# Performance work log

Measured on AMD Instinct MI355X. Metric: run time of the kernel, lower is better.

Reference implementation:

```python
import jax, jax.numpy as jnp
import numpy as np

N, L, D, HEADS = 32, 128, 128, 4
B = 64
MHSA_RESIDUAL = False  # module default


def setup_inputs() -> dict:
    key = jax.random.key(0)
    ks = jax.random.split(key, 21)
    g = lambda k, shape, s=0.05: jax.random.normal(k, shape, dtype=jnp.float32) * s
    return {
        "X": jax.random.normal(ks[0], (B, L, N), dtype=jnp.float32),
        # per-variable encoder LSTM weights, stacked over N (torch gate order i,f,g,o)
        "enc_Wih": g(ks[1], (N, 4 * D)),        # input size is 1 -> (4d,1) squeezed
        "enc_Whh": g(ks[2], (N, 4 * D, D)),
        "enc_bih": g(ks[3], (N, 4 * D)),
        "enc_bhh": g(ks[4], (N, 4 * D)),
        "pool_w": g(ks[5], (N, D)),
        "pool_b": g(ks[6], (N,)),
        # nn.MultiheadAttention packed in-proj + out-proj
        "Wqkv": g(ks[7], (3 * D, D)),
        "bqkv": g(ks[8], (3 * D,)),
        "Wo": g(ks[9], (D, D)),
        "bo": g(ks[10], (D,)),
        # per-variable decoder: init_h/init_c Linear(d, d), LSTM, out Linear(d,1)
        "dec_ih_W": g(ks[11], (N, D, D)),
        "dec_ih_b": g(ks[12], (N, D)),
        "dec_ic_W": g(ks[13], (N, D, D)),
        "dec_ic_b": g(ks[14], (N, D)),
        "dec_Wih": g(ks[15], (N, 4 * D)),       # unused at runtime: decoder input is zeros
        "dec_Whh": g(ks[16], (N, 4 * D, D)),
        "dec_bih": g(ks[17], (N, 4 * D)),
        "dec_bhh": g(ks[18], (N, 4 * D)),
        "dec_out_W": g(ks[19], (N, D)),
        "dec_out_b": g(ks[20], (N,)),
    }


def _lstm_cell(pre, c):
    i, f, g, o = jnp.split(pre, 4, axis=-1)
    c_new = jax.nn.sigmoid(f) * c + jax.nn.sigmoid(i) * jnp.tanh(g)
    h_new = jax.nn.sigmoid(o) * jnp.tanh(c_new)
    return h_new, c_new


def reference(X, enc_Wih, enc_Whh, enc_bih, enc_bhh, pool_w, pool_b,
              Wqkv, bqkv, Wo, bo,
              dec_ih_W, dec_ih_b, dec_ic_W, dec_ic_b,
              dec_Wih, dec_Whh, dec_bih, dec_bhh, dec_out_W, dec_out_b):
    Bx = X.shape[0]
    # ---- N per-variable LSTM encoders, batched over the N axis ----
    x_enc = jnp.transpose(X[:, :L - 1, :], (1, 2, 0))  # (L-1, N, B)
    h0 = jnp.zeros((N, Bx, D), X.dtype)

    def enc_step(carry, x_t):
        h, c = carry
        pre = (x_t[..., None] * enc_Wih[:, None, :]
               + jnp.einsum('nbd,ngd->nbg', h, enc_Whh)
               + (enc_bih + enc_bhh)[:, None, :])
        h, c = _lstm_cell(pre, c)
        return (h, c), h

    _, H = jax.lax.scan(enc_step, (h0, h0), x_enc)  # (L-1, N, B, D)

    # temporal attention pooling (softmax over time)
    s = jnp.einsum('tnbd,nd->tnb', H, pool_w) + pool_b[None, :, None]
    a = jax.nn.softmax(s, axis=0)
    C = jnp.transpose(jnp.einsum('tnb,tnbd->nbd', a, H), (1, 0, 2))  # (B, N, D)

    # ---- MHSA over the variable axis ----
    qkv = C @ Wqkv.T + bqkv  # (B, N, 3D)
    q, k, v = jnp.split(qkv, 3, axis=-1)
    dh = D // HEADS
    split = lambda t: t.reshape(Bx, N, HEADS, dh).transpose(0, 2, 1, 3)  # (B,h,N,dh)
    q, k, v = split(q), split(k), split(v)
    attn = jax.nn.softmax(jnp.einsum('bhqd,bhkd->bhqk', q, k) / jnp.sqrt(jnp.float32(dh)), axis=-1)
    A = jnp.einsum('bhqk,bhkd->bhqd', attn, v).transpose(0, 2, 1, 3).reshape(Bx, N, D)
    A = A @ Wo.T + bo
    C_star = C + A if MHSA_RESIDUAL else A  # (B, N, D)

    # ---- N per-variable LSTM decoders, batched over the N axis ----
    cs = jnp.transpose(C_star, (1, 0, 2))  # (N, B, D)
    h = jnp.tanh(jnp.einsum('nbd,ned->nbe', cs, dec_ih_W) + dec_ih_b[:, None, :])
    c = jnp.tanh(jnp.einsum('nbd,ned->nbe', cs, dec_ic_W) + dec_ic_b[:, None, :])

    def dec_step(carry, _):
        h, c = carry
        # decoder input is identically zero -> W_ih contributes nothing
        pre = jnp.einsum('nbd,ngd->nbg', h, dec_Whh) + (dec_bih + dec_bhh)[:, None, :]
        h, c = _lstm_cell(pre, c)
        return (h, c), h

    _, Y = jax.lax.scan(dec_step, (h, c), None, length=L)  # (L, N, B, D)
    O = jnp.einsum('lnbd,nd->lnb', Y, dec_out_W) + dec_out_b[None, :, None]  # (L, N, B)
    recon = jnp.transpose(O[:L - 1], (2, 0, 1))  # (B, L-1, N)
    pred = O[L - 1].T                             # (B, N)
    return recon, pred, C_star
```

## Files before the change

### kernel.cpp

```cpp
#include <hip/hip_runtime.h>


typedef _Float16 h8  __attribute__((ext_vector_type(8)));
typedef _Float16 h4v __attribute__((ext_vector_type(4)));
typedef float    f4  __attribute__((ext_vector_type(4)));
typedef float    f2v __attribute__((ext_vector_type(2)));

#define DI __device__ __forceinline__

constexpr int NV  = 32;
constexpr int LT  = 128;
constexpr int DH  = 128;
constexpr int GG  = 4 * DH;
constexpr int BR  = 8;
constexpr int NW  = 8;
constexpr int TPB = NW * 64;
constexpr int HSTR = DH + 8;
constexpr float LOG2E = 1.4426950408889634f;

DI float rcp_(float x) { return __builtin_amdgcn_rcpf(x); }
DI float ex2_(float x) { return __builtin_amdgcn_exp2f(x); }

DI float tanh_(float x) {
    float xc = fminf(fmaxf(x, -20.0f), 20.0f);
    float E = ex2_(2.0f * LOG2E * xc);
    return (E - 1.0f) * rcp_(E + 1.0f);
}

DI float lstm_cell(float iv, float fv, float gv, float ov, float& c) {
    float Ai = ex2_(iv);
    float Af = ex2_(fv);
    float Bg = ex2_(gv);
    float ai1 = 1.0f + Ai, af1 = 1.0f + Af, bg1 = 1.0f + Bg;
    float P = ai1 * bg1;
    float N = fmaf(c, P, (Bg - 1.0f) * af1);
    c = N * rcp_(P * af1);
    float cc = fminf(fmaxf(c, -20.0f), 20.0f);
    float Ec = ex2_(2.0f * LOG2E * cc);
    float Eo = ex2_(ov);
    return (Ec - 1.0f) * rcp_((1.0f + Eo) * (1.0f + Ec));
}

DI h8 cvt8(f4 a, f4 b) {
    h8 r;
    r[0] = (_Float16)a[0]; r[1] = (_Float16)a[1];
    r[2] = (_Float16)a[2]; r[3] = (_Float16)a[3];
    r[4] = (_Float16)b[0]; r[5] = (_Float16)b[1];
    r[6] = (_Float16)b[2]; r[7] = (_Float16)b[3];
    return r;
}
DI h8 cvt8s(f4 a, f4 b, float s) {
    h8 r;
    r[0] = (_Float16)(a[0] * s); r[1] = (_Float16)(a[1] * s);
    r[2] = (_Float16)(a[2] * s); r[3] = (_Float16)(a[3] * s);
    r[4] = (_Float16)(b[0] * s); r[5] = (_Float16)(b[1] * s);
    r[6] = (_Float16)(b[2] * s); r[7] = (_Float16)(b[3] * s);
    return r;
}

__constant__ float GSC[4] = {-LOG2E, -LOG2E, 2.0f * LOG2E, -LOG2E};

__global__ __launch_bounds__(TPB, 2)
void enc_kernel(const float* __restrict__ X,
                const float* __restrict__ Wih,
                const float* __restrict__ Whh,
                const float* __restrict__ bih,
                const float* __restrict__ bhh,
                const float* __restrict__ poolw,
                float* __restrict__ Cout)
{
    const int n    = blockIdx.x & 31;
    const int b0   = (blockIdx.x >> 5) * BR;
    const int tid  = threadIdx.x;
    const int wv   = tid >> 6;
    const int lane = tid & 63;
    const int quad = lane >> 4;
    const int l16  = lane & 15;
    const int dmy  = wv * 16 + l16;

    __shared__ _Float16 hbuf[2][16 * HSTR];
    __shared__ float xs[(LT - 1) * BR];
    __shared__ float pfin[2][BR];

    h8 Wf[4][4];
    float wihr[4];
    f4 bsp[4];
#pragma unroll
    for (int g4 = 0; g4 < 4; ++g4) {
        const float s = GSC[g4];
        const int g = g4 * DH + dmy;
        const float* wrow = Whh + (size_t)(n * GG + g) * DH;
#pragma unroll
        for (int kc = 0; kc < 4; ++kc) {
            f4 w0 = *(const f4*)(wrow + kc * 32 + quad * 8);
            f4 w1 = *(const f4*)(wrow + kc * 32 + quad * 8 + 4);
            Wf[g4][kc] = cvt8s(w0, w1, s);
        }
        wihr[g4] = Wih[n * GG + g] * s;
        const float bb = (bih[n * GG + g] + bhh[n * GG + g]) * s;
        bsp[g4] = (f4){bb, bb, bb, bb};
    }
    h8 Bp[4];
#pragma unroll
    for (int kc = 0; kc < 4; ++kc) {
        if (l16 == 0) {
            f4 p0 = *(const f4*)(poolw + n * DH + kc * 32 + quad * 8);
            f4 p1 = *(const f4*)(poolw + n * DH + kc * 32 + quad * 8 + 4);
            Bp[kc] = cvt8s(p0, p1, LOG2E);
        } else {
            Bp[kc] = (h8)(_Float16)0.0f;
        }
    }

    for (int i = tid; i < (LT - 1) * BR; i += TPB)
        xs[i] = X[((size_t)(b0 + (i & 7)) * LT + (i >> 3)) * NV + n];
    for (int i = tid; i < 2 * 16 * HSTR; i += TPB)
        ((_Float16*)hbuf)[i] = (_Float16)0.0f;
    __syncthreads();

    float cst[2]   = {0.f, 0.f};
    float lsum[2]  = {0.f, 0.f};
    float acc[2]   = {0.f, 0.f};
    float hprev[2] = {0.f, 0.f};

    for (int t = 0; t < LT - 1; ++t) {
        const _Float16* hb = hbuf[t & 1];
        h8 a[4];
#pragma unroll
        for (int kc = 0; kc < 4; ++kc)
            a[kc] = *(const h8*)(hb + l16 * HSTR + kc * 32 + quad * 8);

        f4 pre[4];
#pragma unroll
        for (int g4 = 0; g4 < 4; ++g4)
            pre[g4] = __builtin_amdgcn_mfma_f32_16x16x32_f16(
                a[0], Wf[g4][0], bsp[g4], 0, 0, 0);
#pragma unroll
        for (int kc = 1; kc < 4; ++kc)
#pragma unroll
            for (int g4 = 0; g4 < 4; ++g4)
                pre[g4] = __builtin_amdgcn_mfma_f32_16x16x32_f16(
                    a[kc], Wf[g4][kc], pre[g4], 0, 0, 0);

        if (wv == 0) {
            f4 sp = {0.f, 0.f, 0.f, 0.f};
#pragma unroll
            for (int kc = 0; kc < 4; ++kc)
                sp = __builtin_amdgcn_mfma_f32_16x16x32_f16(a[kc], Bp[kc], sp, 0, 0, 0);
            if (l16 == 0) {
                pfin[t & 1][quad * 2 + 0] = ex2_(sp[0]);
                pfin[t & 1][quad * 2 + 1] = ex2_(sp[1]);
            }
        }

        const f2v xv = *(const f2v*)(xs + t * BR + quad * 2);
        float hv[2];
#pragma unroll
        for (int r = 0; r < 2; ++r) {
            hv[r] = lstm_cell(fmaf(xv[r], wihr[0], pre[0][r]),
                              fmaf(xv[r], wihr[1], pre[1][r]),
                              fmaf(xv[r], wihr[2], pre[2][r]),
                              fmaf(xv[r], wihr[3], pre[3][r]), cst[r]);
        }

        _Float16* hn = hbuf[(t + 1) & 1];
#pragma unroll
        for (int r = 0; r < 2; ++r)
            hn[(quad * 4 + r) * HSTR + dmy] = (_Float16)hv[r];
        __syncthreads();

        if (t > 0) {
#pragma unroll
            for (int r = 0; r < 2; ++r) {
                const float p = pfin[t & 1][quad * 2 + r];
                lsum[r] += p;
                acc[r] = fmaf(p, hprev[r], acc[r]);
            }
        }
#pragma unroll
        for (int r = 0; r < 2; ++r) hprev[r] = hv[r];
    }

    if (wv == 0) {
        const _Float16* hb = hbuf[(LT - 1) & 1];
        h8 a[4];
#pragma unroll
        for (int kc = 0; kc < 4; ++kc)
            a[kc] = *(const h8*)(hb + l16 * HSTR + kc * 32 + quad * 8);
        f4 sp = {0.f, 0.f, 0.f, 0.f};
#pragma unroll
        for (int kc = 0; kc < 4; ++kc)
            sp = __builtin_amdgcn_mfma_f32_16x16x32_f16(a[kc], Bp[kc], sp, 0, 0, 0);
        if (l16 == 0) {
            pfin[(LT - 1) & 1][quad * 2 + 0] = ex2_(sp[0]);
            pfin[(LT - 1) & 1][quad * 2 + 1] = ex2_(sp[1]);
        }
    }
    __syncthreads();
#pragma unroll
    for (int r = 0; r < 2; ++r) {
        const float p = pfin[(LT - 1) & 1][quad * 2 + r];
        lsum[r] += p;
        acc[r] = fmaf(p, hprev[r], acc[r]);
    }
#pragma unroll
    for (int r = 0; r < 2; ++r) {
        const int b = b0 + quad * 2 + r;
        Cout[((size_t)b * NV + n) * DH + dmy] = acc[r] * rcp_(lsum[r]);
    }
}

constexpr int CS2 = DH + 8;
constexpr int QS  = 40;

__global__ __launch_bounds__(256)
void attn_kernel(const float* __restrict__ Cin,
                 const float* __restrict__ Wqkv,
                 const float* __restrict__ bqkv,
                 float* __restrict__ Astage)
{
    const int b    = blockIdx.x >> 2;
    const int hh   = blockIdx.x & 3;
    const int tid  = threadIdx.x;
    const int wv   = tid >> 6;
    const int lane = tid & 63;
    const int quad = lane >> 4;
    const int l16  = lane & 15;

    __shared__ _Float16 Cb[NV][CS2];
    __shared__ _Float16 qs[NV][QS], ks[NV][QS], vT[NV][QS];
    __shared__ float    S[NV][NV + 1];
    __shared__ _Float16 P[NV][QS];

    for (int i = tid; i < NV * DH / 4; i += 256) {
        const int nn = i >> 5, d4 = (i & 31) * 4;
        f4 v = *(const f4*)(Cin + ((size_t)b * NV + nn) * DH + d4);
        h4v hv4;
        hv4[0] = (_Float16)v[0]; hv4[1] = (_Float16)v[1];
        hv4[2] = (_Float16)v[2]; hv4[3] = (_Float16)v[3];
        *(h4v*)(&Cb[nn][d4]) = hv4;
    }
    __syncthreads();

    const int m0 = (wv >> 1) * 16;
    const int n0 = (wv & 1) * 16;

    h8 a[4];
#pragma unroll
    for (int kc = 0; kc < 4; ++kc)
        a[kc] = *(const h8*)(&Cb[m0 + l16][kc * 32 + quad * 8]);

#pragma unroll
    for (int mat = 0; mat < 3; ++mat) {
        const int rbase = mat * DH + hh * 32;
        const float* wrow = Wqkv + (size_t)(rbase + n0 + l16) * DH;
        const float bias  = bqkv[rbase + n0 + l16];
        f4 acc = {bias, bias, bias, bias};
#pragma unroll
        for (int kc = 0; kc < 4; ++kc) {
            f4 w0 = *(const f4*)(wrow + kc * 32 + quad * 8);
            f4 w1 = *(const f4*)(wrow + kc * 32 + quad * 8 + 4);
            acc = __builtin_amdgcn_mfma_f32_16x16x32_f16(a[kc], cvt8(w0, w1), acc, 0, 0, 0);
        }
#pragma unroll
        for (int r = 0; r < 4; ++r) {
            const int tok = m0 + quad * 4 + r, col = n0 + l16;
            if (mat == 0)      qs[tok][col] = (_Float16)acc[r];
            else if (mat == 1) ks[tok][col] = (_Float16)acc[r];
            else               vT[col][tok] = (_Float16)acc[r];
        }
    }
    __syncthreads();

    {
        h8 aq = *(const h8*)(&qs[m0 + l16][quad * 8]);
        h8 bk = *(const h8*)(&ks[n0 + l16][quad * 8]);
        f4 sc = {0.f, 0.f, 0.f, 0.f};
        sc = __builtin_amdgcn_mfma_f32_16x16x32_f16(aq, bk, sc, 0, 0, 0);
#pragma unroll
        for (int r = 0; r < 4; ++r)
            S[m0 + quad * 4 + r][n0 + l16] = sc[r] * 0.17677669529663687f;
    }
    __syncthreads();

    if (tid < NV) {
        float mx = -1e30f;
        for (int j = 0; j < NV; ++j) mx = fmaxf(mx, S[tid][j]);
        float l = 0.0f;
        float p[NV];
#pragma unroll
        for (int j = 0; j < NV; ++j) {
            p[j] = ex2_(LOG2E * (S[tid][j] - mx));
            l += p[j];
        }
        const float rl = rcp_(l);
#pragma unroll
        for (int j = 0; j < NV; ++j) P[tid][j] = (_Float16)(p[j] * rl);
    }
    __syncthreads();

    {
        h8 ap = *(const h8*)(&P[m0 + l16][quad * 8]);
        h8 bv = *(const h8*)(&vT[n0 + l16][quad * 8]);
        f4 av = {0.f, 0.f, 0.f, 0.f};
        av = __builtin_amdgcn_mfma_f32_16x16x32_f16(ap, bv, av, 0, 0, 0);
#pragma unroll
        for (int r = 0; r < 4; ++r) {
            const int tok = m0 + quad * 4 + r;
            Astage[((size_t)b * NV + tok) * DH + hh * 32 + n0 + l16] = av[r];
        }
    }
}

__global__ __launch_bounds__(256)
void outproj_kernel(const float* __restrict__ Wo,
                    const float* __restrict__ bo,
                    float* __restrict__ AC)
{
    const int mb   = blockIdx.x * 16;
    const int tid  = threadIdx.x;
    const int wv   = tid >> 6;
    const int lane = tid & 63;
    const int quad = lane >> 4;
    const int l16  = lane & 15;

    __shared__ _Float16 As[16][HSTR];

    for (int i = tid; i < 16 * DH / 4; i += 256) {
        const int rr = i >> 5, d4 = (i & 31) * 4;
        f4 v = *(const f4*)(AC + ((size_t)(mb + rr)) * DH + d4);
        h4v hv4;
        hv4[0] = (_Float16)v[0]; hv4[1] = (_Float16)v[1];
        hv4[2] = (_Float16)v[2]; hv4[3] = (_Float16)v[3];
        *(h4v*)(&As[rr][d4]) = hv4;
    }
    __syncthreads();

    h8 a[4];
#pragma unroll
    for (int kc = 0; kc < 4; ++kc)
        a[kc] = *(const h8*)(&As[l16][kc * 32 + quad * 8]);

#pragma unroll
    for (int i = 0; i < 2; ++i) {
        const int n0 = (wv * 2 + i) * 16;
        const float* wrow = Wo + (size_t)(n0 + l16) * DH;
        const float bias  = bo[n0 + l16];
        f4 acc = {bias, bias, bias, bias};
#pragma unroll
        for (int kc = 0; kc < 4; ++kc) {
            f4 w0 = *(const f4*)(wrow + kc * 32 + quad * 8);
            f4 w1 = *(const f4*)(wrow + kc * 32 + quad * 8 + 4);
            acc = __builtin_amdgcn_mfma_f32_16x16x32_f16(a[kc], cvt8(w0, w1), acc, 0, 0, 0);
        }
#pragma unroll
        for (int r = 0; r < 4; ++r)
            AC[((size_t)(mb + quad * 4 + r)) * DH + n0 + l16] = acc[r];
    }
}

__global__ __launch_bounds__(TPB, 2)
void dec_kernel(const float* __restrict__ Cstar,
                const float* __restrict__ ihW,
                const float* __restrict__ ihb,
                const float* __restrict__ icW,
                const float* __restrict__ icb,
                const float* __restrict__ Whh,
                const float* __restrict__ bih,
                const float* __restrict__ bhh,
                const float* __restrict__ outW,
                const float* __restrict__ outb,
                float* __restrict__ recon,
                float* __restrict__ pred)
{
    const int n    = blockIdx.x & 31;
    const int b0   = (blockIdx.x >> 5) * BR;
    const int tid  = threadIdx.x;
    const int wv   = tid >> 6;
    const int lane = tid & 63;
    const int quad = lane >> 4;
    const int l16  = lane & 15;
    const int dmy  = wv * 16 + l16;

    __shared__ _Float16 hbuf[2][16 * HSTR];
    __shared__ float obuf[LT - 1][BR];

    h8 Wf[4][4];
    f4 bsp[4];
#pragma unroll
    for (int g4 = 0; g4 < 4; ++g4) {
        const float s = GSC[g4];
        const int g = g4 * DH + dmy;
        const float* wrow = Whh + (size_t)(n * GG + g) * DH;
#pragma unroll
        for (int kc = 0; kc < 4; ++kc) {
            f4 w0 = *(const f4*)(wrow + kc * 32 + quad * 8);
            f4 w1 = *(const f4*)(wrow + kc * 32 + quad * 8 + 4);
            Wf[g4][kc] = cvt8s(w0, w1, s);
        }
        const float bb = (bih[n * GG + g] + bhh[n * GG + g]) * s;
        bsp[g4] = (f4){bb, bb, bb, bb};
    }
    h8 Bo[4];
#pragma unroll
    for (int kc = 0; kc < 4; ++kc) {
        if (l16 == 0) {
            f4 p0 = *(const f4*)(outW + n * DH + kc * 32 + quad * 8);
            f4 p1 = *(const f4*)(outW + n * DH + kc * 32 + quad * 8 + 4);
            Bo[kc] = cvt8(p0, p1);
        } else {
            Bo[kc] = (h8)(_Float16)0.0f;
        }
    }
    const float ob = outb[n];

    for (int i = tid; i < 2 * 16 * HSTR; i += TPB)
        ((_Float16*)hbuf)[i] = (_Float16)0.0f;
    __syncthreads();
    if (tid < 256) {
        const int j = tid >> 5, d4 = (tid & 31) * 4;
        const int row = (j >> 1) * 4 + (j & 1);
        f4 v = *(const f4*)(Cstar + ((size_t)(b0 + j) * NV + n) * DH + d4);
        h4v hv4;
        hv4[0] = (_Float16)v[0]; hv4[1] = (_Float16)v[1];
        hv4[2] = (_Float16)v[2]; hv4[3] = (_Float16)v[3];
        *(h4v*)(&hbuf[0][row * HSTR + d4]) = hv4;
    }
    __syncthreads();

    float cst[2], hv0[2];
    {
        h8 a[4];
#pragma unroll
        for (int kc = 0; kc < 4; ++kc)
            a[kc] = *(const h8*)(hbuf[0] + l16 * HSTR + kc * 32 + quad * 8);
        const float bh = ihb[n * DH + dmy];
        const float bc = icb[n * DH + dmy];
        f4 Ph = {bh, bh, bh, bh};
        f4 Pc = {bc, bc, bc, bc};
        const float* hrow = ihW + (size_t)(n * DH + dmy) * DH;
        const float* crow = icW + (size_t)(n * DH + dmy) * DH;
#pragma unroll
        for (int kc = 0; kc < 4; ++kc) {
            f4 w0 = *(const f4*)(hrow + kc * 32 + quad * 8);
            f4 w1 = *(const f4*)(hrow + kc * 32 + quad * 8 + 4);
            Ph = __builtin_amdgcn_mfma_f32_16x16x32_f16(a[kc], cvt8(w0, w1), Ph, 0, 0, 0);
            f4 u0 = *(const f4*)(crow + kc * 32 + quad * 8);
            f4 u1 = *(const f4*)(crow + kc * 32 + quad * 8 + 4);
            Pc = __builtin_amdgcn_mfma_f32_16x16x32_f16(a[kc], cvt8(u0, u1), Pc, 0, 0, 0);
        }
#pragma unroll
        for (int r = 0; r < 2; ++r) {
            hv0[r] = tanh_(Ph[r]);
            cst[r] = tanh_(Pc[r]);
        }
    }
    __syncthreads();
#pragma unroll
    for (int r = 0; r < 2; ++r)
        hbuf[0][(quad * 4 + r) * HSTR + dmy] = (_Float16)hv0[r];
    __syncthreads();

    for (int t = 0; t < LT; ++t) {
        const _Float16* hb = hbuf[t & 1];
        h8 a[4];
#pragma unroll
        for (int kc = 0; kc < 4; ++kc)
            a[kc] = *(const h8*)(hb + l16 * HSTR + kc * 32 + quad * 8);

        f4 pre[4];
#pragma unroll
        for (int g4 = 0; g4 < 4; ++g4)
            pre[g4] = __builtin_amdgcn_mfma_f32_16x16x32_f16(
                a[0], Wf[g4][0], bsp[g4], 0, 0, 0);
#pragma unroll
        for (int kc = 1; kc < 4; ++kc)
#pragma unroll
            for (int g4 = 0; g4 < 4; ++g4)
                pre[g4] = __builtin_amdgcn_mfma_f32_16x16x32_f16(
                    a[kc], Wf[g4][kc], pre[g4], 0, 0, 0);

        if (wv == 0 && t > 0) {
            f4 so = {0.f, 0.f, 0.f, 0.f};
#pragma unroll
            for (int kc = 0; kc < 4; ++kc)
                so = __builtin_amdgcn_mfma_f32_16x16x32_f16(a[kc], Bo[kc], so, 0, 0, 0);
            if (l16 == 0) {
                obuf[t - 1][quad * 2 + 0] = so[0] + ob;
                obuf[t - 1][quad * 2 + 1] = so[1] + ob;
            }
        }

        float hv[2];
#pragma unroll
        for (int r = 0; r < 2; ++r)
            hv[r] = lstm_cell(pre[0][r], pre[1][r], pre[2][r], pre[3][r], cst[r]);

        _Float16* hn = hbuf[(t + 1) & 1];
#pragma unroll
        for (int r = 0; r < 2; ++r)
            hn[(quad * 4 + r) * HSTR + dmy] = (_Float16)hv[r];
        __syncthreads();
    }

    if (wv == 0) {
        const _Float16* hb = hbuf[LT & 1];
        h8 a[4];
#pragma unroll
        for (int kc = 0; kc < 4; ++kc)
            a[kc] = *(const h8*)(hb + l16 * HSTR + kc * 32 + quad * 8);
        f4 so = {0.f, 0.f, 0.f, 0.f};
#pragma unroll
        for (int kc = 0; kc < 4; ++kc)
            so = __builtin_amdgcn_mfma_f32_16x16x32_f16(a[kc], Bo[kc], so, 0, 0, 0);
        if (l16 == 0) {
            pred[(size_t)(b0 + quad * 2 + 0) * NV + n] = so[0] + ob;
            pred[(size_t)(b0 + quad * 2 + 1) * NV + n] = so[1] + ob;
        }
    }

    if (tid < LT - 1) {
#pragma unroll
        for (int b = 0; b < BR; ++b)
            recon[((size_t)(b0 + b) * (LT - 1) + tid) * NV + n] = obuf[tid][b];
    }
}

extern "C" void kernel_launch(void* const* d_in, const int* in_sizes, int n_in,
                              void* d_out, int out_size, void* d_ws, size_t ws_size,
                              hipStream_t stream) {
    (void)in_sizes; (void)n_in; (void)d_ws; (void)ws_size; (void)out_size;

    const float* X     = (const float*)d_in[0];
    const float* eWih  = (const float*)d_in[1];
    const float* eWhh  = (const float*)d_in[2];
    const float* ebih  = (const float*)d_in[3];
    const float* ebhh  = (const float*)d_in[4];
    const float* poolw = (const float*)d_in[5];
    const float* Wqkv  = (const float*)d_in[7];
    const float* bqkv  = (const float*)d_in[8];
    const float* Wo    = (const float*)d_in[9];
    const float* bo    = (const float*)d_in[10];
    const float* dihW  = (const float*)d_in[11];
    const float* dihb  = (const float*)d_in[12];
    const float* dicW  = (const float*)d_in[13];
    const float* dicb  = (const float*)d_in[14];
    const float* dWhh  = (const float*)d_in[16];
    const float* dbih  = (const float*)d_in[17];
    const float* dbhh  = (const float*)d_in[18];
    const float* doutW = (const float*)d_in[19];
    const float* doutb = (const float*)d_in[20];

    float* out   = (float*)d_out;
    float* recon = out;
    float* pred  = out + 64 * 127 * 32;
    float* Cstar = out + 64 * 127 * 32 + 64 * 32;
    float* Cpool = out;

    enc_kernel<<<dim3(256), dim3(TPB), 0, stream>>>(
        X, eWih, eWhh, ebih, ebhh, poolw, Cpool);
    attn_kernel<<<dim3(256), dim3(256), 0, stream>>>(
        Cpool, Wqkv, bqkv, Cstar);
    outproj_kernel<<<dim3(128), dim3(256), 0, stream>>>(
        Wo, bo, Cstar);
    dec_kernel<<<dim3(256), dim3(TPB), 0, stream>>>(
        Cstar, dihW, dihb, dicW, dicb, dWhh, dbih, dbhh,
        doutW, doutb, recon, pred);
}
```

Before: 292.8 us.

## Fuse encoder, attention, out-proj and decoder into one persistent kernel with grid barriers

Merges the four separate launches into a single 256-block kernel that steps through each stage and uses atomic-counter grid barriers in the workspace between them. Shared memory is carved from one aliased buffer reused by each phase. The aim is to remove launch gaps and tail effects between kernels. In exchange, attention now runs with 512-thread blocks where half the threads idle, and a memset is added. Correctness depends on all 256 blocks being co-resident, or the barrier deadlocks.

After: 347.3 us. +18.6%, slower.

```diff
diff --git a/kernel.cpp b/kernel.cpp
--- a/kernel.cpp
+++ b/kernel.cpp
@@ -16,7 +16,21 @@
 constexpr int NW  = 8;
 constexpr int TPB = NW * 64;
 constexpr int HSTR = DH + 8;
+constexpr int NBLK = 256;
 constexpr float LOG2E = 1.4426950408889634f;
+
+constexpr int CS2 = DH + 8;
+constexpr int QS  = 40;
+
+constexpr int SM_HBUF = 0;
+constexpr int SM_XS   = 8704;
+constexpr int SM_PFIN = 8704 + 4064;
+constexpr int SM_QS   = 8704;
+constexpr int SM_KS   = 8704 + 2560;
+constexpr int SM_VT   = 8704 + 5120;
+constexpr int SM_S    = 8704 + 7680;
+constexpr int SM_P    = 8704 + 7680 + 4224;
+constexpr int SM_SZ   = 23424;
 
 DI float rcp_(float x) { return __builtin_amdgcn_rcpf(x); }
 DI float ex2_(float x) { return __builtin_amdgcn_exp2f(x); }
@@ -60,17 +74,47 @@
 
 __constant__ float GSC[4] = {-LOG2E, -LOG2E, 2.0f * LOG2E, -LOG2E};
 
+DI void gsync(unsigned* bar, int k) {
+    __syncthreads();
+    if (threadIdx.x == 0) {
+        __threadfence();
+        atomicAdd(bar + k, 1u);
+        while (atomicAdd(bar + k, 0u) < (unsigned)NBLK)
+            __builtin_amdgcn_s_sleep(2);
+        __threadfence();
+    }
+    __syncthreads();
+}
+
 __global__ __launch_bounds__(TPB, 2)
-void enc_kernel(const float* __restrict__ X,
-                const float* __restrict__ Wih,
-                const float* __restrict__ Whh,
-                const float* __restrict__ bih,
-                const float* __restrict__ bhh,
-                const float* __restrict__ poolw,
-                float* __restrict__ Cout)
+void fused_kernel(const float* __restrict__ X,
+                  const float* __restrict__ Wih,
+                  const float* __restrict__ Whh,
+                  const float* __restrict__ bih,
+                  const float* __restrict__ bhh,
+                  const float* __restrict__ poolw,
+                  const float* __restrict__ Wqkv,
+                  const float* __restrict__ bqkv,
+                  const float* __restrict__ Wo,
+                  const float* __restrict__ bo,
+                  const float* __restrict__ ihW,
+                  const float* __restrict__ ihb,
+                  const float* __restrict__ icW,
+                  const float* __restrict__ icb,
+                  const float* __restrict__ dWhh,
+                  const float* __restrict__ dbih,
+                  const float* __restrict__ dbhh,
+                  const float* __restrict__ outW,
+                  const float* __restrict__ outb,
+                  float* __restrict__ Cpool,
+                  float* __restrict__ Cstar,
+                  float* __restrict__ recon,
+                  float* __restrict__ pred,
+                  unsigned* __restrict__ bar)
 {
-    const int n    = blockIdx.x & 31;
-    const int b0   = (blockIdx.x >> 5) * BR;
+    __shared__ __align__(16) char smem[SM_SZ];
+
+    const int blk  = blockIdx.x;
     const int tid  = threadIdx.x;
     const int wv   = tid >> 6;
     const int lane = tid & 63;
@@ -78,183 +122,260 @@
     const int l16  = lane & 15;
     const int dmy  = wv * 16 + l16;
 
-    __shared__ _Float16 hbuf[2][16 * HSTR];
-    __shared__ float xs[(LT - 1) * BR];
-    __shared__ float pfin[2][BR];
-
-    h8 Wf[4][4];
-    float wihr[4];
-    f4 bsp[4];
-#pragma unroll
-    for (int g4 = 0; g4 < 4; ++g4) {
-        const float s = GSC[g4];
-        const int g = g4 * DH + dmy;
-        const float* wrow = Whh + (size_t)(n * GG + g) * DH;
+    {
+        const int n  = blk & 31;
+        const int b0 = (blk >> 5) * BR;
+
+        _Float16 (*hbuf)[16 * HSTR] = (_Float16(*)[16 * HSTR])(smem + SM_HBUF);
+        float* xs = (float*)(smem + SM_XS);
+        float (*pfin)[BR] = (float(*)[BR])(smem + SM_PFIN);
+
+        h8 Wf[4][4];
+        float wihr[4];
+        f4 bsp[4];
+#pragma unroll
+        for (int g4 = 0; g4 < 4; ++g4) {
+            const float s = GSC[g4];
+            const int g = g4 * DH + dmy;
+            const float* wrow = Whh + (size_t)(n * GG + g) * DH;
+#pragma unroll
+            for (int kc = 0; kc < 4; ++kc) {
+                f4 w0 = *(const f4*)(wrow + kc * 32 + quad * 8);
+                f4 w1 = *(const f4*)(wrow + kc * 32 + quad * 8 + 4);
+                Wf[g4][kc] = cvt8s(w0, w1, s);
+            }
+            wihr[g4] = Wih[n * GG + g] * s;
+            const float bb = (bih[n * GG + g] + bhh[n * GG + g]) * s;
+            bsp[g4] = (f4){bb, bb, bb, bb};
+        }
+        h8 Bp[4];
 #pragma unroll
         for (int kc = 0; kc < 4; ++kc) {
-            f4 w0 = *(const f4*)(wrow + kc * 32 + quad * 8);
-            f4 w1 = *(const f4*)(wrow + kc * 32 + quad * 8 + 4);
-            Wf[g4][kc] = cvt8s(w0, w1, s);
-        }
-        wihr[g4] = Wih[n * GG + g] * s;
-        const float bb = (bih[n * GG + g] + bhh[n * GG + g]) * s;
-        bsp[g4] = (f4){bb, bb, bb, bb};
-    }
-    h8 Bp[4];
-#pragma unroll
-    for (int kc = 0; kc < 4; ++kc) {
-        if (l16 == 0) {
-            f4 p0 = *(const f4*)(poolw + n * DH + kc * 32 + quad * 8);
-            f4 p1 = *(const f4*)(poolw + n * DH + kc * 32 + quad * 8 + 4);
-            Bp[kc] = cvt8s(p0, p1, LOG2E);
-        } else {
-            Bp[kc] = (h8)(_Float16)0.0f;
-        }
-    }
-
-    for (int i = tid; i < (LT - 1) * BR; i += TPB)
-        xs[i] = X[((size_t)(b0 + (i & 7)) * LT + (i >> 3)) * NV + n];
-    for (int i = tid; i < 2 * 16 * HSTR; i += TPB)
-        ((_Float16*)hbuf)[i] = (_Float16)0.0f;
-    __syncthreads();
-
-    float cst[2]   = {0.f, 0.f};
-    float lsum[2]  = {0.f, 0.f};
-    float acc[2]   = {0.f, 0.f};
-    float hprev[2] = {0.f, 0.f};
-
-    for (int t = 0; t < LT - 1; ++t) {
-        const _Float16* hb = hbuf[t & 1];
-        h8 a[4];
-#pragma unroll
-        for (int kc = 0; kc < 4; ++kc)
-            a[kc] = *(const h8*)(hb + l16 * HSTR + kc * 32 + quad * 8);
-
-        f4 pre[4];
-#pragma unroll
-        for (int g4 = 0; g4 < 4; ++g4)
-            pre[g4] = __builtin_amdgcn_mfma_f32_16x16x32_f16(
-                a[0], Wf[g4][0], bsp[g4], 0, 0, 0);
-#pragma unroll
-        for (int kc = 1; kc < 4; ++kc)
+            if (l16 == 0) {
+                f4 p0 = *(const f4*)(poolw + n * DH + kc * 32 + quad * 8);
+                f4 p1 = *(const f4*)(poolw + n * DH + kc * 32 + quad * 8 + 4);
+                Bp[kc] = cvt8s(p0, p1, LOG2E);
+            } else {
+                Bp[kc] = (h8)(_Float16)0.0f;
+            }
+        }
+
+        for (int i = tid; i < (LT - 1) * BR; i += TPB)
+            xs[i] = X[((size_t)(b0 + (i & 7)) * LT + (i >> 3)) * NV + n];
+        for (int i = tid; i < 2 * 16 * HSTR; i += TPB)
+            ((_Float16*)hbuf)[i] = (_Float16)0.0f;
+        __syncthreads();
+
+        float cst[2]   = {0.f, 0.f};
+        float lsum[2]  = {0.f, 0.f};
+        float acc[2]   = {0.f, 0.f};
+        float hprev[2] = {0.f, 0.f};
+
+        for (int t = 0; t < LT - 1; ++t) {
+            const _Float16* hb = hbuf[t & 1];
+            h8 a[4];
+#pragma unroll
+            for (int kc = 0; kc < 4; ++kc)
+                a[kc] = *(const h8*)(hb + l16 * HSTR + kc * 32 + quad * 8);
+
+            f4 pre[4];
 #pragma unroll
             for (int g4 = 0; g4 < 4; ++g4)
                 pre[g4] = __builtin_amdgcn_mfma_f32_16x16x32_f16(
-                    a[kc], Wf[g4][kc], pre[g4], 0, 0, 0);
+                    a[0], Wf[g4][0], bsp[g4], 0, 0, 0);
+#pragma unroll
+            for (int kc = 1; kc < 4; ++kc)
+#pragma unroll
+                for (int g4 = 0; g4 < 4; ++g4)
+                    pre[g4] = __builtin_amdgcn_mfma_f32_16x16x32_f16(
+                        a[kc], Wf[g4][kc], pre[g4], 0, 0, 0);
+
+            if (wv == 0) {
+                f4 sp = {0.f, 0.f, 0.f, 0.f};
+#pragma unroll
+                for (int kc = 0; kc < 4; ++kc)
+                    sp = __builtin_amdgcn_mfma_f32_16x16x32_f16(a[kc], Bp[kc], sp, 0, 0, 0);
+                if (l16 == 0) {
+                    pfin[t & 1][quad * 2 + 0] = ex2_(sp[0]);
+                    pfin[t & 1][quad * 2 + 1] = ex2_(sp[1]);
+                }
+            }
+
+            const f2v xv = *(const f2v*)(xs + t * BR + quad * 2);
+            float hv[2];
+#pragma unroll
+            for (int r = 0; r < 2; ++r) {
+                hv[r] = lstm_cell(fmaf(xv[r], wihr[0], pre[0][r]),
+                                  fmaf(xv[r], wihr[1], pre[1][r]),
+                                  fmaf(xv[r], wihr[2], pre[2][r]),
+                                  fmaf(xv[r], wihr[3], pre[3][r]), cst[r]);
+            }
+
+            _Float16* hn = hbuf[(t + 1) & 1];
+#pragma unroll
+            for (int r = 0; r < 2; ++r)
+                hn[(quad * 4 + r) * HSTR + dmy] = (_Float16)hv[r];
+            __syncthreads();
+
+            if (t > 0) {
+#pragma unroll
+                for (int r = 0; r < 2; ++r) {
+                    const float p = pfin[t & 1][quad * 2 + r];
+                    lsum[r] += p;
+                    acc[r] = fmaf(p, hprev[r], acc[r]);
+                }
+            }
+#pragma unroll
+            for (int r = 0; r < 2; ++r) hprev[r] = hv[r];
+        }
 
         if (wv == 0) {
+            const _Float16* hb = hbuf[(LT - 1) & 1];
+            h8 a[4];
+#pragma unroll
+            for (int kc = 0; kc < 4; ++kc)
+                a[kc] = *(const h8*)(hb + l16 * HSTR + kc * 32 + quad * 8);
             f4 sp = {0.f, 0.f, 0.f, 0.f};
 #pragma unroll
             for (int kc = 0; kc < 4; ++kc)
                 sp = __builtin_amdgcn_mfma_f32_16x16x32_f16(a[kc], Bp[kc], sp, 0, 0, 0);
             if (l16 == 0) {
-                pfin[t & 1][quad * 2 + 0] = ex2_(sp[0]);
-                pfin[t & 1][quad * 2 + 1] = ex2_(sp[1]);
-            }
-        }
-
-        const f2v xv = *(const f2v*)(xs + t * BR + quad * 2);
-        float hv[2];
+                pfin[(LT - 1) & 1][quad * 2 + 0] = ex2_(sp[0]);
+                pfin[(LT - 1) & 1][quad * 2 + 1] = ex2_(sp[1]);
+            }
+        }
+        __syncthreads();
 #pragma unroll
         for (int r = 0; r < 2; ++r) {
-            hv[r] = lstm_cell(fmaf(xv[r], wihr[0], pre[0][r]),
-                              fmaf(xv[r], wihr[1], pre[1][r]),
-                              fmaf(xv[r], wihr[2], pre[2][r]),
-                              fmaf(xv[r], wihr[3], pre[3][r]), cst[r]);
-        }
-
-        _Float16* hn = hbuf[(t + 1) & 1];
-#pragma unroll
-        for (int r = 0; r < 2; ++r)
-            hn[(quad * 4 + r) * HSTR + dmy] = (_Float16)hv[r];
-        __syncthreads();
-
-        if (t > 0) {
-#pragma unroll
-            for (int r = 0; r < 2; ++r) {
-                const float p = pfin[t & 1][quad * 2 + r];
-                lsum[r] += p;
-                acc[r] = fmaf(p, hprev[r], acc[r]);
-            }
-        }
-#pragma unroll
-        for (int r = 0; r < 2; ++r) hprev[r] = hv[r];
+            const float p = pfin[(LT - 1) & 1][quad * 2 + r];
+            lsum[r] += p;
+            acc[r] = fmaf(p, hprev[r], acc[r]);
+        }
+#pragma unroll
+        for (int r = 0; r < 2; ++r) {
+            const int b = b0 + quad * 2 + r;
+            Cpool[((size_t)b * NV + n) * DH + dmy] = acc[r] * rcp_(lsum[r]);
+        }
     }
 
-    if (wv == 0) {
-        const _Float16* hb = hbuf[(LT - 1) & 1];
+    gsync(bar, 0);
+
+    {
+        const int b  = blk >> 2;
+        const int hh = blk & 3;
+
+        _Float16 (*Cb)[CS2] = (_Float16(*)[CS2])(smem + SM_HBUF);
+        _Float16 (*qs)[QS]  = (_Float16(*)[QS])(smem + SM_QS);
+        _Float16 (*ks)[QS]  = (_Float16(*)[QS])(smem + SM_KS);
+        _Float16 (*vT)[QS]  = (_Float16(*)[QS])(smem + SM_VT);
+        float    (*S)[NV+1] = (float(*)[NV+1])(smem + SM_S);
+        _Float16 (*P)[QS]   = (_Float16(*)[QS])(smem + SM_P);
+
+        for (int i = tid; i < NV * DH / 4; i += TPB) {
+            const int nn = i >> 5, d4 = (i & 31) * 4;
+            f4 v = *(const f4*)(Cpool + ((size_t)b * NV + nn) * DH + d4);
+            h4v hv4;
+            hv4[0] = (_Float16)v[0]; hv4[1] = (_Float16)v[1];
+            hv4[2] = (_Float16)v[2]; hv4[3] = (_Float16)v[3];
+            *(h4v*)(&Cb[nn][d4]) = hv4;
+        }
+        __syncthreads();
+
+        const int m0 = ((wv & 3) >> 1) * 16;
+        const int n0 = (wv & 1) * 16;
+
+        if (tid < 256) {
+            h8 a[4];
+#pragma unroll
+            for (int kc = 0; kc < 4; ++kc)
+                a[kc] = *(const h8*)(&Cb[m0 + l16][kc * 32 + quad * 8]);
+#pragma unroll
+            for (int mat = 0; mat < 3; ++mat) {
+                const int rbase = mat * DH + hh * 32;
+                const float* wrow = Wqkv + (size_t)(rbase + n0 + l16) * DH;
+                const float bias  = bqkv[rbase + n0 + l16];
+                f4 acc = {bias, bias, bias, bias};
+#pragma unroll
+                for (int kc = 0; kc < 4; ++kc) {
+                    f4 w0 = *(const f4*)(wrow + kc * 32 + quad * 8);
+                    f4 w1 = *(const f4*)(wrow + kc * 32 + quad * 8 + 4);
+                    acc = __builtin_amdgcn_mfma_f32_16x16x32_f16(a[kc], cvt8(w0, w1), acc, 0, 0, 0);
+                }
+#pragma unroll
+                for (int r = 0; r < 4; ++r) {
+                    const int tok = m0 + quad * 4 + r, col = n0 + l16;
+                    if (mat == 0)      qs[tok][col] = (_Float16)acc[r];
+                    else if (mat == 1) ks[tok][col] = (_Float16)acc[r];
+                    else               vT[col][tok] = (_Float16)acc[r];
+                }
+            }
+        }
+        __syncthreads();
+
+        if (tid < 256) {
+            h8 aq = *(const h8*)(&qs[m0 + l16][quad * 8]);
+            h8 bk = *(const h8*)(&ks[n0 + l16][quad * 8]);
+            f4 sc = {0.f, 0.f, 0.f, 0.f};
+            sc = __builtin_amdgcn_mfma_f32_16x16x32_f16(aq, bk, sc, 0, 0, 0);
+#pragma unroll
+            for (int r = 0; r < 4; ++r)
+                S[m0 + quad * 4 + r][n0 + l16] = sc[r] * 0.17677669529663687f;
+        }
+        __syncthreads();
+
+        if (tid < NV) {
+            float mx = -1e30f;
+            for (int j = 0; j < NV; ++j) mx = fmaxf(mx, S[tid][j]);
+            float l = 0.0f;
+            float p[NV];
+#pragma unroll
+            for (int j = 0; j < NV; ++j) {
+                p[j] = ex2_(LOG2E * (S[tid][j] - mx));
+                l += p[j];
+            }
+            const float rl = rcp_(l);
+#pragma unroll
+            for (int j = 0; j < NV; ++j) P[tid][j] = (_Float16)(p[j] * rl);
+        }
+        __syncthreads();
+
+        if (tid < 256) {
+            h8 ap = *(const h8*)(&P[m0 + l16][quad * 8]);
+            h8 bv = *(const h8*)(&vT[n0 + l16][quad * 8]);
+            f4 av = {0.f, 0.f, 0.f, 0.f};
+            av = __builtin_amdgcn_mfma_f32_16x16x32_f16(ap, bv, av, 0, 0, 0);
+#pragma unroll
+            for (int r = 0; r < 4; ++r) {
+                const int tok = m0 + quad * 4 + r;
+                Cstar[((size_t)b * NV + tok) * DH + hh * 32 + n0 + l16] = av[r];
+            }
+        }
+    }
+
+    gsync(bar, 1);
+
+    if (blk < 128) {
+        const int mb = blk * 16;
+        _Float16 (*As)[HSTR] = (_Float16(*)[HSTR])(smem + SM_HBUF);
+
+        {
+            const int rr = tid >> 5, d4 = (tid & 31) * 4;
+            f4 v = *(const f4*)(Cstar + ((size_t)(mb + rr)) * DH + d4);
+            h4v hv4;
+            hv4[0] = (_Float16)v[0]; hv4[1] = (_Float16)v[1];
+            hv4[2] = (_Float16)v[2]; hv4[3] = (_Float16)v[3];
+            *(h4v*)(&As[rr][d4]) = hv4;
+        }
+        __syncthreads();
+
         h8 a[4];
 #pragma unroll
         for (int kc = 0; kc < 4; ++kc)
-            a[kc] = *(const h8*)(hb + l16 * HSTR + kc * 32 + quad * 8);
-        f4 sp = {0.f, 0.f, 0.f, 0.f};
-#pragma unroll
-        for (int kc = 0; kc < 4; ++kc)
-            sp = __builtin_amdgcn_mfma_f32_16x16x32_f16(a[kc], Bp[kc], sp, 0, 0, 0);
-        if (l16 == 0) {
-            pfin[(LT - 1) & 1][quad * 2 + 0] = ex2_(sp[0]);
-            pfin[(LT - 1) & 1][quad * 2 + 1] = ex2_(sp[1]);
-        }
-    }
-    __syncthreads();
-#pragma unroll
-    for (int r = 0; r < 2; ++r) {
-        const float p = pfin[(LT - 1) & 1][quad * 2 + r];
-        lsum[r] += p;
-        acc[r] = fmaf(p, hprev[r], acc[r]);
-    }
-#pragma unroll
-    for (int r = 0; r < 2; ++r) {
-        const int b = b0 + quad * 2 + r;
-        Cout[((size_t)b * NV + n) * DH + dmy] = acc[r] * rcp_(lsum[r]);
-    }
-}
-
-constexpr int CS2 = DH + 8;
-constexpr int QS  = 40;
-
-__global__ __launch_bounds__(256)
-void attn_kernel(const float* __restrict__ Cin,
-                 const float* __restrict__ Wqkv,
-                 const float* __restrict__ bqkv,
-                 float* __restrict__ Astage)
-{
-    const int b    = blockIdx.x >> 2;
-    const int hh   = blockIdx.x & 3;
-    const int tid  = threadIdx.x;
-    const int wv   = tid >> 6;
-    const int lane = tid & 63;
-    const int quad = lane >> 4;
-    const int l16  = lane & 15;
-
-    __shared__ _Float16 Cb[NV][CS2];
-    __shared__ _Float16 qs[NV][QS], ks[NV][QS], vT[NV][QS];
-    __shared__ float    S[NV][NV + 1];
-    __shared__ _Float16 P[NV][QS];
-
-    for (int i = tid; i < NV * DH / 4; i += 256) {
-        const int nn = i >> 5, d4 = (i & 31) * 4;
-        f4 v = *(const f4*)(Cin + ((size_t)b * NV + nn) * DH + d4);
-        h4v hv4;
-        hv4[0] = (_Float16)v[0]; hv4[1] = (_Float16)v[1];
-        hv4[2] = (_Float16)v[2]; hv4[3] = (_Float16)v[3];
-        *(h4v*)(&Cb[nn][d4]) = hv4;
-    }
-    __syncthreads();
-
-    const int m0 = (wv >> 1) * 16;
-    const int n0 = (wv & 1) * 16;
-
-    h8 a[4];
-#pragma unroll
-    for (int kc = 0; kc < 4; ++kc)
-        a[kc] = *(const h8*)(&Cb[m0 + l16][kc * 32 + quad * 8]);
-
-#pragma unroll
-    for (int mat = 0; mat < 3; ++mat) {
-        const int rbase = mat * DH + hh * 32;
-        const float* wrow = Wqkv + (size_t)(rbase + n0 + l16) * DH;
-        const float bias  = bqkv[rbase + n0 + l16];
+            a[kc] = *(const h8*)(&As[l16][kc * 32 + quad * 8]);
+
+        const int n0 = wv * 16;
+        const float* wrow = Wo + (size_t)(n0 + l16) * DH;
+        const float bias  = bo[n0 + l16];
         f4 acc = {bias, bias, bias, bias};
 #pragma unroll
         for (int kc = 0; kc < 4; ++kc) {
@@ -263,273 +384,165 @@
             acc = __builtin_amdgcn_mfma_f32_16x16x32_f16(a[kc], cvt8(w0, w1), acc, 0, 0, 0);
         }
 #pragma unroll
-        for (int r = 0; r < 4; ++r) {
-            const int tok = m0 + quad * 4 + r, col = n0 + l16;
-            if (mat == 0)      qs[tok][col] = (_Float16)acc[r];
-            else if (mat == 1) ks[tok][col] = (_Float16)acc[r];
-            else               vT[col][tok] = (_Float16)acc[r];
-        }
+        for (int r = 0; r < 4; ++r)
+            Cstar[((size_t)(mb + quad * 4 + r)) * DH + n0 + l16] = acc[r];
     }
-    __syncthreads();
+
+    gsync(bar, 2);
 
     {
-        h8 aq = *(const h8*)(&qs[m0 + l16][quad * 8]);
-        h8 bk = *(const h8*)(&ks[n0 + l16][quad * 8]);
-        f4 sc = {0.f, 0.f, 0.f, 0.f};
-        sc = __builtin_amdgcn_mfma_f32_16x16x32_f16(aq, bk, sc, 0, 0, 0);
-#pragma unroll
-        for (int r = 0; r < 4; ++r)
-            S[m0 + quad * 4 + r][n0 + l16] = sc[r] * 0.17677669529663687f;
-    }
-    __syncthreads();
-
-    if (tid < NV) {
-        float mx = -1e30f;
-        for (int j = 0; j < NV; ++j) mx = fmaxf(mx, S[tid][j]);
-        float l = 0.0f;
-        float p[NV];
-#pragma unroll
-        for (int j = 0; j < NV; ++j) {
-            p[j] = ex2_(LOG2E * (S[tid][j] - mx));
-            l += p[j];
-        }
-        const float rl = rcp_(l);
-#pragma unroll
-        for (int j = 0; j < NV; ++j) P[tid][j] = (_Float16)(p[j] * rl);
-    }
-    __syncthreads();
-
-    {
-        h8 ap = *(const h8*)(&P[m0 + l16][quad * 8]);
-        h8 bv = *(const h8*)(&vT[n0 + l16][quad * 8]);
-        f4 av = {0.f, 0.f, 0.f, 0.f};
-        av = __builtin_amdgcn_mfma_f32_16x16x32_f16(ap, bv, av, 0, 0, 0);
-#pragma unroll
-        for (int r = 0; r < 4; ++r) {
-            const int tok = m0 + quad * 4 + r;
-            Astage[((size_t)b * NV + tok) * DH + hh * 32 + n0 + l16] = av[r];
-        }
-    }
-}
-
-__global__ __launch_bounds__(256)
-void outproj_kernel(const float* __restrict__ Wo,
-                    const float* __restrict__ bo,
-                    float* __restrict__ AC)
-{
-    const int mb   = blockIdx.x * 16;
-    const int tid  = threadIdx.x;
-    const int wv   = tid >> 6;
-    const int lane = tid & 63;
-    const int quad = lane >> 4;
-    const int l16  = lane & 15;
-
-    __shared__ _Float16 As[16][HSTR];
-
-    for (int i = tid; i < 16 * DH / 4; i += 256) {
-        const int rr = i >> 5, d4 = (i & 31) * 4;
-        f4 v = *(const f4*)(AC + ((size_t)(mb + rr)) * DH + d4);
-        h4v hv4;
-        hv4[0] = (_Float16)v[0]; hv4[1] = (_Float16)v[1];
-        hv4[2] = (_Float16)v[2]; hv4[3] = (_Float16)v[3];
-        *(h4v*)(&As[rr][d4]) = hv4;
-    }
-    __syncthreads();
-
-    h8 a[4];
-#pragma unroll
-    for (int kc = 0; kc < 4; ++kc)
-        a[kc] = *(const h8*)(&As[l16][kc * 32 + quad * 8]);
-
-#pragma unroll
-    for (int i = 0; i < 2; ++i) {
-        const int n0 = (wv * 2 + i) * 16;
-        const float* wrow = Wo + (size_t)(n0 + l16) * DH;
-        const float bias  = bo[n0 + l16];
-        f4 acc = {bias, bias, bias, bias};
+        const int n  = blk & 31;
+        const int b0 = (blk >> 5) * BR;
+
+        _Float16 (*hbuf)[16 * HSTR] = (_Float16(*)[16 * HSTR])(smem + SM_HBUF);
+        float (*obuf)[BR] = (float(*)[BR])(smem + SM_XS);
+
+        h8 Wf[4][4];
+        f4 bsp[4];
+#pragma unroll
+        for (int g4 = 0; g4 < 4; ++g4) {
+            const float s = GSC[g4];
+            const int g = g4 * DH + dmy;
+            const float* wrow = dWhh + (size_t)(n * GG + g) * DH;
+#pragma unroll
+            for (int kc = 0; kc < 4; ++kc) {
+                f4 w0 = *(const f4*)(wrow + kc * 32 + quad * 8);
+                f4 w1 = *(const f4*)(wrow + kc * 32 + quad * 8 + 4);
+                Wf[g4][kc] = cvt8s(w0, w1, s);
+            }
+            const float bb = (dbih[n * GG + g] + dbhh[n * GG + g]) * s;
+            bsp[g4] = (f4){bb, bb, bb, bb};
+        }
+        h8 Bo[4];
 #pragma unroll
         for (int kc = 0; kc < 4; ++kc) {
-            f4 w0 = *(const f4*)(wrow + kc * 32 + quad * 8);
-            f4 w1 = *(const f4*)(wrow + kc * 32 + quad * 8 + 4);
-            acc = __builtin_amdgcn_mfma_f32_16x16x32_f16(a[kc], cvt8(w0, w1), acc, 0, 0, 0);
-        }
-#pragma unroll
-        for (int r = 0; r < 4; ++r)
-            AC[((size_t)(mb + quad * 4 + r)) * DH + n0 + l16] = acc[r];
-    }
-}
-
-__global__ __launch_bounds__(TPB, 2)
-void dec_kernel(const float* __restrict__ Cstar,
-                const float* __restrict__ ihW,
-                const float* __restrict__ ihb,
-                const float* __restrict__ icW,
-                const float* __restrict__ icb,
-                const float* __restrict__ Whh,
-                const float* __restrict__ bih,
-                const float* __restrict__ bhh,
-                const float* __restrict__ outW,
-                const float* __restrict__ outb,
-                float* __restrict__ recon,
-                float* __restrict__ pred)
-{
-    const int n    = blockIdx.x & 31;
-    const int b0   = (blockIdx.x >> 5) * BR;
-    const int tid  = threadIdx.x;
-    const int wv   = tid >> 6;
-    const int lane = tid & 63;
-    const int quad = lane >> 4;
-    const int l16  = lane & 15;
-    const int dmy  = wv * 16 + l16;
-
-    __shared__ _Float16 hbuf[2][16 * HSTR];
-    __shared__ float obuf[LT - 1][BR];
-
-    h8 Wf[4][4];
-    f4 bsp[4];
-#pragma unroll
-    for (int g4 = 0; g4 < 4; ++g4) {
-        const float s = GSC[g4];
-        const int g = g4 * DH + dmy;
-        const float* wrow = Whh + (size_t)(n * GG + g) * DH;
-#pragma unroll
-        for (int kc = 0; kc < 4; ++kc) {
-            f4 w0 = *(const f4*)(wrow + kc * 32 + quad * 8);
-            f4 w1 = *(const f4*)(wrow + kc * 32 + quad * 8 + 4);
-            Wf[g4][kc] = cvt8s(w0, w1, s);
-        }
-        const float bb = (bih[n * GG + g] + bhh[n * GG + g]) * s;
-        bsp[g4] = (f4){bb, bb, bb, bb};
-    }
-    h8 Bo[4];
-#pragma unroll
-    for (int kc = 0; kc < 4; ++kc) {
-        if (l16 == 0) {
-            f4 p0 = *(const f4*)(outW + n * DH + kc * 32 + quad * 8);
-            f4 p1 = *(const f4*)(outW + n * DH + kc * 32 + quad * 8 + 4);
-            Bo[kc] = cvt8(p0, p1);
-        } else {
-            Bo[kc] = (h8)(_Float16)0.0f;
-        }
-    }
-    const float ob = outb[n];
-
-    for (int i = tid; i < 2 * 16 * HSTR; i += TPB)
-        ((_Float16*)hbuf)[i] = (_Float16)0.0f;
-    __syncthreads();
-    if (tid < 256) {
-        const int j = tid >> 5, d4 = (tid & 31) * 4;
-        const int row = (j >> 1) * 4 + (j & 1);
-        f4 v = *(const f4*)(Cstar + ((size_t)(b0 + j) * NV + n) * DH + d4);
-        h4v hv4;
-        hv4[0] = (_Float16)v[0]; hv4[1] = (_Float16)v[1];
-        hv4[2] = (_Float16)v[2]; hv4[3] = (_Float16)v[3];
-        *(h4v*)(&hbuf[0][row * HSTR + d4]) = hv4;
-    }
-    __syncthreads();
-
-    float cst[2], hv0[2];
-    {
-        h8 a[4];
-#pragma unroll
-        for (int kc = 0; kc < 4; ++kc)
-            a[kc] = *(const h8*)(hbuf[0] + l16 * HSTR + kc * 32 + quad * 8);
-        const float bh = ihb[n * DH + dmy];
-        const float bc = icb[n * DH + dmy];
-        f4 Ph = {bh, bh, bh, bh};
-        f4 Pc = {bc, bc, bc, bc};
-        const float* hrow = ihW + (size_t)(n * DH + dmy) * DH;
-        const float* crow = icW + (size_t)(n * DH + dmy) * DH;
-#pragma unroll
-        for (int kc = 0; kc < 4; ++kc) {
-            f4 w0 = *(const f4*)(hrow + kc * 32 + quad * 8);
-            f4 w1 = *(const f4*)(hrow + kc * 32 + quad * 8 + 4);
-            Ph = __builtin_amdgcn_mfma_f32_16x16x32_f16(a[kc], cvt8(w0, w1), Ph, 0, 0, 0);
-            f4 u0 = *(const f4*)(crow + kc * 32 + quad * 8);
-            f4 u1 = *(const f4*)(crow + kc * 32 + quad * 8 + 4);
-            Pc = __builtin_amdgcn_mfma_f32_16x16x32_f16(a[kc], cvt8(u0, u1), Pc, 0, 0, 0);
-        }
-#pragma unroll
-        for (int r = 0; r < 2; ++r) {
-            hv0[r] = tanh_(Ph[r]);
-            cst[r] = tanh_(Pc[r]);
-        }
-    }
-    __syncthreads();
-#pragma unroll
-    for (int r = 0; r < 2; ++r)
-        hbuf[0][(quad * 4 + r) * HSTR + dmy] = (_Float16)hv0[r];
-    __syncthreads();
-
-    for (int t = 0; t < LT; ++t) {
-        const _Float16* hb = hbuf[t & 1];
-        h8 a[4];
-#pragma unroll
-        for (int kc = 0; kc < 4; ++kc)
-            a[kc] = *(const h8*)(hb + l16 * HSTR + kc * 32 + quad * 8);
-
-        f4 pre[4];
-#pragma unroll
-        for (int g4 = 0; g4 < 4; ++g4)
-            pre[g4] = __builtin_amdgcn_mfma_f32_16x16x32_f16(
-                a[0], Wf[g4][0], bsp[g4], 0, 0, 0);
-#pragma unroll
-        for (int kc = 1; kc < 4; ++kc)
+            if (l16 == 0) {
+                f4 p0 = *(const f4*)(outW + n * DH + kc * 32 + quad * 8);
+                f4 p1 = *(const f4*)(outW + n * DH + kc * 32 + quad * 8 + 4);
+                Bo[kc] = cvt8(p0, p1);
+            } else {
+                Bo[kc] = (h8)(_Float16)0.0f;
+            }
+        }
+        const float ob = outb[n];
+
+        for (int i = tid; i < 2 * 16 * HSTR; i += TPB)
+            ((_Float16*)hbuf)[i] = (_Float16)0.0f;
+        __syncthreads();
+        if (tid < 256) {
+            const int j = tid >> 5, d4 = (tid & 31) * 4;
+            const int row = (j >> 1) * 4 + (j & 1);
+            f4 v = *(const f4*)(Cstar + ((size_t)(b0 + j) * NV + n) * DH + d4);
+            h4v hv4;
+            hv4[0] = (_Float16)v[0]; hv4[1] = (_Float16)v[1];
+            hv4[2] = (_Float16)v[2]; hv4[3] = (_Float16)v[3];
+            *(h4v*)(&hbuf[0][row * HSTR + d4]) = hv4;
+        }
+        __syncthreads();
+
+        float cst[2], hv0[2];
+        {
+            h8 a[4];
+#pragma unroll
+            for (int kc = 0; kc < 4; ++kc)
+                a[kc] = *(const h8*)(hbuf[0] + l16 * HSTR + kc * 32 + quad * 8);
+            const float bh = ihb[n * DH + dmy];
+            const float bc = icb[n * DH + dmy];
+            f4 Ph = {bh, bh, bh, bh};
+            f4 Pc = {bc, bc, bc, bc};
+            const float* hrow = ihW + (size_t)(n * DH + dmy) * DH;
+            const float* crow = icW + (size_t)(n * DH + dmy) * DH;
+#pragma unroll
+            for (int kc = 0; kc < 4; ++kc) {
+                f4 w0 = *(const f4*)(hrow + kc * 32 + quad * 8);
+                f4 w1 = *(const f4*)(hrow + kc * 32 + quad * 8 + 4);
+                Ph = __builtin_amdgcn_mfma_f32_16x16x32_f16(a[kc], cvt8(w0, w1), Ph, 0, 0, 0);
+                f4 u0 = *(const f4*)(crow + kc * 32 + quad * 8);
+                f4 u1 = *(const f4*)(crow + kc * 32 + quad * 8 + 4);
+                Pc = __builtin_amdgcn_mfma_f32_16x16x32_f16(a[kc], cvt8(u0, u1), Pc, 0, 0, 0);
+            }
+#pragma unroll
+            for (int r = 0; r < 2; ++r) {
+                hv0[r] = tanh_(Ph[r]);
+                cst[r] = tanh_(Pc[r]);
+            }
+        }
+        __syncthreads();
+#pragma unroll
+        for (int r = 0; r < 2; ++r)
+            hbuf[0][(quad * 4 + r) * HSTR + dmy] = (_Float16)hv0[r];
+        __syncthreads();
+
+        for (int t = 0; t < LT; ++t) {
+            const _Float16* hb = hbuf[t & 1];
+            h8 a[4];
+#pragma unroll
+            for (int kc = 0; kc < 4; ++kc)
+                a[kc] = *(const h8*)(hb + l16 * HSTR + kc * 32 + quad * 8);
+
+            f4 pre[4];
 #pragma unroll
             for (int g4 = 0; g4 < 4; ++g4)
                 pre[g4] = __builtin_amdgcn_mfma_f32_16x16x32_f16(
-                    a[kc], Wf[g4][kc], pre[g4], 0, 0, 0);
-
-        if (wv == 0 && t > 0) {
+                    a[0], Wf[g4][0], bsp[g4], 0, 0, 0);
+#pragma unroll
+            for (int kc = 1; kc < 4; ++kc)
+#pragma unroll
+                for (int g4 = 0; g4 < 4; ++g4)
+                    pre[g4] = __builtin_amdgcn_mfma_f32_16x16x32_f16(
+                        a[kc], Wf[g4][kc], pre[g4], 0, 0, 0);
+
+            if (wv == 0 && t > 0) {
+                f4 so = {0.f, 0.f, 0.f, 0.f};
+#pragma unroll
+                for (int kc = 0; kc < 4; ++kc)
+                    so = __builtin_amdgcn_mfma_f32_16x16x32_f16(a[kc], Bo[kc], so, 0, 0, 0);
+                if (l16 == 0) {
+                    obuf[t - 1][quad * 2 + 0] = so[0] + ob;
+                    obuf[t - 1][quad * 2 + 1] = so[1] + ob;
+                }
+            }
+
+            float hv[2];
+#pragma unroll
+            for (int r = 0; r < 2; ++r)
+                hv[r] = lstm_cell(pre[0][r], pre[1][r], pre[2][r], pre[3][r], cst[r]);
+
+            _Float16* hn = hbuf[(t + 1) & 1];
+#pragma unroll
+            for (int r = 0; r < 2; ++r)
+                hn[(quad * 4 + r) * HSTR + dmy] = (_Float16)hv[r];
+            __syncthreads();
+        }
+
+        if (wv == 0) {
+            const _Float16* hb = hbuf[LT & 1];
+            h8 a[4];
+#pragma unroll
+            for (int kc = 0; kc < 4; ++kc)
+                a[kc] = *(const h8*)(hb + l16 * HSTR + kc * 32 + quad * 8);
             f4 so = {0.f, 0.f, 0.f, 0.f};
 #pragma unroll
             for (int kc = 0; kc < 4; ++kc)
                 so = __builtin_amdgcn_mfma_f32_16x16x32_f16(a[kc], Bo[kc], so, 0, 0, 0);
             if (l16 == 0) {
-                obuf[t - 1][quad * 2 + 0] = so[0] + ob;
-                obuf[t - 1][quad * 2 + 1] = so[1] + ob;
-            }
-        }
-
-        float hv[2];
-#pragma unroll
-        for (int r = 0; r < 2; ++r)
-            hv[r] = lstm_cell(pre[0][r], pre[1][r], pre[2][r], pre[3][r], cst[r]);
-
-        _Float16* hn = hbuf[(t + 1) & 1];
-#pragma unroll
-        for (int r = 0; r < 2; ++r)
-            hn[(quad * 4 + r) * HSTR + dmy] = (_Float16)hv[r];
-        __syncthreads();
-    }
-
-    if (wv == 0) {
-        const _Float16* hb = hbuf[LT & 1];
-        h8 a[4];
-#pragma unroll
-        for (int kc = 0; kc < 4; ++kc)
-            a[kc] = *(const h8*)(hb + l16 * HSTR + kc * 32 + quad * 8);
-        f4 so = {0.f, 0.f, 0.f, 0.f};
-#pragma unroll
-        for (int kc = 0; kc < 4; ++kc)
-            so = __builtin_amdgcn_mfma_f32_16x16x32_f16(a[kc], Bo[kc], so, 0, 0, 0);
-        if (l16 == 0) {
-            pred[(size_t)(b0 + quad * 2 + 0) * NV + n] = so[0] + ob;
-            pred[(size_t)(b0 + quad * 2 + 1) * NV + n] = so[1] + ob;
-        }
-    }
-
-    if (tid < LT - 1) {
-#pragma unroll
-        for (int b = 0; b < BR; ++b)
-            recon[((size_t)(b0 + b) * (LT - 1) + tid) * NV + n] = obuf[tid][b];
+                pred[(size_t)(b0 + quad * 2 + 0) * NV + n] = so[0] + ob;
+                pred[(size_t)(b0 + quad * 2 + 1) * NV + n] = so[1] + ob;
+            }
+        }
+
+        if (tid < LT - 1) {
+#pragma unroll
+            for (int b = 0; b < BR; ++b)
+                recon[((size_t)(b0 + b) * (LT - 1) + tid) * NV + n] = obuf[tid][b];
+        }
     }
 }
 
 extern "C" void kernel_launch(void* const* d_in, const int* in_sizes, int n_in,
                               void* d_out, int out_size, void* d_ws, size_t ws_size,
                               hipStream_t stream) {
-    (void)in_sizes; (void)n_in; (void)d_ws; (void)ws_size; (void)out_size;
+    (void)in_sizes; (void)n_in; (void)ws_size; (void)out_size;
 
     const float* X     = (const float*)d_in[0];
     const float* eWih  = (const float*)d_in[1];
@@ -557,13 +570,13 @@
     float* Cstar = out + 64 * 127 * 32 + 64 * 32;
     float* Cpool = out;
 
-    enc_kernel<<<dim3(256), dim3(TPB), 0, stream>>>(
-        X, eWih, eWhh, ebih, ebhh, poolw, Cpool);
-    attn_kernel<<<dim3(256), dim3(256), 0, stream>>>(
-        Cpool, Wqkv, bqkv, Cstar);
-    outproj_kernel<<<dim3(128), dim3(256), 0, stream>>>(
-        Wo, bo, Cstar);
-    dec_kernel<<<dim3(256), dim3(TPB), 0, stream>>>(
-        Cstar, dihW, dihb, dicW, dicb, dWhh, dbih, dbhh,
-        doutW, doutb, recon, pred);
-}
+    unsigned* bar = (unsigned*)d_ws;
+    hipMemsetAsync(bar, 0, 4 * sizeof(unsigned), stream);
+
+    fused_kernel<<<dim3(NBLK), dim3(TPB), 0, stream>>>(
+        X, eWih, eWhh, ebih, ebhh, poolw,
+        Wqkv, bqkv, Wo, bo,
+        dihW, dihb, dicW, dicb,
+        dWhh, dbih, dbhh, doutW, doutb,
+        Cpool, Cstar, recon, pred, bar);
+}
```
